# Kernel tuning notes

Hardware: AMD Instinct MI355X
Metric: run time of the kernel (lower is better)

The kernel has to match this reference:

```python
import jax, jax.numpy as jnp
import numpy as np

B, L1, L2, H = 8, 384, 384, 128


def _lin(k, out_f, in_f, scale=0.05):
    kw, kb = jax.random.split(k)
    return (jax.random.normal(kw, (out_f, in_f), jnp.float32) * scale,
            jax.random.normal(kb, (out_f,), jnp.float32) * scale)


def setup_inputs() -> dict:
    key = jax.random.key(0)
    ks = jax.random.split(key, 10)
    Wq_w, Wq_b = _lin(ks[2], H, H)
    Wup_w, Wup_b = _lin(ks[3], H, H)
    Wvp_w, Wvp_b = _lin(ks[4], H, H)
    V_w, V_b = _lin(ks[5], 1, H)
    Wg_w, Wg_b = _lin(ks[6], 2 * H, 2 * H)
    W_ih, b_ih = _lin(ks[7], 4 * H, 2 * H)
    W_hh, b_hh = _lin(ks[8], 4 * H, H)
    return {
        "x": jax.random.normal(ks[0], (B, L1, H), jnp.float32),
        "x_mask": jnp.zeros((B, L1), dtype=bool),
        "y": jax.random.normal(ks[1], (B, L2, H), jnp.float32),
        "y_mask": jnp.zeros((B, L2), dtype=bool),
        "Wq_w": Wq_w, "Wq_b": Wq_b,
        "Wup_w": Wup_w, "Wup_b": Wup_b,
        "Wvp_w": Wvp_w, "Wvp_b": Wvp_b,
        "V_w": V_w, "V_b": V_b,
        "Wg_w": Wg_w, "Wg_b": Wg_b,
        "W_ih": W_ih, "W_hh": W_hh, "b_ih": b_ih, "b_hh": b_hh,
    }


def reference(x, x_mask, y, y_mask, Wq_w, Wq_b, Wup_w, Wup_b, Wvp_w, Wvp_b,
              V_w, V_b, Wg_w, Wg_b, W_ih, W_hh, b_ih, b_hh):
    b, l1, h = x.shape
    # projections (torch Linear: x @ W.T + b)
    x_proj = x @ Wup_w.T + Wup_b                      # [B, L1, H]
    y_proj = y @ Wq_w.T + Wq_b                        # [B, L2, H]
    # source feeds a constant zero hidden state into W_vp -> just its bias
    hidden_proj = jnp.zeros((h,), x.dtype) @ Wvp_w.T + Wvp_b  # [H]
    # additive attention scores: V . tanh(xp + yp + hp)
    sum_batch = jnp.tanh(x_proj[:, :, None, :] + y_proj[:, None, :, :] + hidden_proj)  # [B,L1,L2,H]
    s = jnp.einsum('btjh,h->btj', sum_batch, V_w[0]) + V_b[0]  # [B, L1, L2]
    # sum_mask = (1 - x_mask) outer (1 - y_mask)
    xm = 1.0 - x_mask.astype(s.dtype)
    ym = 1.0 - y_mask.astype(s.dtype)
    s = s * (xm[:, :, None] * ym[:, None, :])
    s = jnp.where(y_mask[:, None, :], -jnp.inf, s)
    alpha = jax.nn.softmax(s, axis=-1)                # [B, L1, L2]
    ct = jnp.einsum('btj,bjh->bth', alpha, y)         # [B, L1, H]
    merge = jnp.concatenate([x, ct], axis=2)          # [B, L1, 2H]
    gt = jax.nn.sigmoid(merge @ Wg_w.T + Wg_b)
    lstm_in = gt * merge                              # [B, L1, 2H]
    # single-layer unidirectional LSTM (torch gate order: i, f, g, o)
    gates_x = lstm_in @ W_ih.T + b_ih                 # [B, L1, 4H]

    def step(carry, gx):
        h_t, c_t = carry
        g = gx + h_t @ W_hh.T + b_hh
        i, f, gg, o = jnp.split(g, 4, axis=-1)
        c_n = jax.nn.sigmoid(f) * c_t + jax.nn.sigmoid(i) * jnp.tanh(gg)
        h_n = jax.nn.sigmoid(o) * jnp.tanh(c_n)
        return (h_n, c_n), h_n

    init = (jnp.zeros((b, h), x.dtype), jnp.zeros((b, h), x.dtype))
    _, hs = jax.lax.scan(step, init, jnp.swapaxes(gates_x, 0, 1))  # [L1, B, H]
    return jnp.swapaxes(hs, 0, 1)                     # [B, L1, H]
```

## Files before the change

kernel.cpp:

```cpp
#include <hip/hip_runtime.h>
#include <hip/hip_bf16.h>
#include <math.h>

typedef __attribute__((ext_vector_type(4))) float  float4v;
typedef __attribute__((ext_vector_type(2))) float  float2v;
typedef __attribute__((ext_vector_type(8))) short  short8;

#define B_ 8
#define L_ 384
#define H_ 128

__device__ __forceinline__ float bflo(unsigned int u){ unsigned int t = u << 16; float f; __builtin_memcpy(&f,&t,4); return f; }
__device__ __forceinline__ unsigned short f2bf(float f){
  unsigned int t; __builtin_memcpy(&t,&f,4);
  return (unsigned short)((t + 0x7fffu + ((t>>16)&1u)) >> 16);
}
__device__ __forceinline__ float fsig(float x){ return __fdividef(1.f, 1.f + __expf(-x)); }

__device__ __forceinline__ void barrier_lds(){
  asm volatile("s_waitcnt lgkmcnt(0)\n\ts_barrier" ::: "memory");
}

template<int K>
__device__ __forceinline__ void mfma_rowgemm_body(
    unsigned short* in_s,
    const float* __restrict__ inA, const float* __restrict__ inB,
    const float* __restrict__ W, const float* __restrict__ bias,
    const float* __restrict__ bias2, float* __restrict__ out,
    int Ntotal, int act, int row0, int ob)
{
  constexpr int KP = K + 2;
  const int tid  = threadIdx.x;
  const int w    = tid >> 6;
  const int l    = tid & 63;
  const int c    = l & 15;
  const int quad = l >> 4;

  #pragma unroll
  for (int it = 0; it < K/32; ++it) {
    int idx = it*256 + tid;
    int r = idx / (K/4);
    int k = (idx % (K/4)) * 4;
    float4v f;
    if (inB != nullptr && k >= 128)
      f = *(const float4v*)(inB + (size_t)(row0+r)*128 + (k-128));
    else if (inB != nullptr)
      f = *(const float4v*)(inA + (size_t)(row0+r)*128 + k);
    else
      f = *(const float4v*)(inA + (size_t)(row0+r)*K + k);
    unsigned int p0 = (unsigned int)f2bf(f.x) | ((unsigned int)f2bf(f.y) << 16);
    unsigned int p1 = (unsigned int)f2bf(f.z) | ((unsigned int)f2bf(f.w) << 16);
    *(unsigned int*)&in_s[r*KP + k]     = p0;
    *(unsigned int*)&in_s[r*KP + k + 2] = p1;
  }

  const int n = ob + w*16 + c;
  short8 bfr[K/32];
  #pragma unroll
  for (int kt = 0; kt < K/32; ++kt) {
    const float* src = W + (size_t)n*K + kt*32 + quad*8;
    float4v f0 = *(const float4v*)(src);
    float4v f1 = *(const float4v*)(src + 4);
    short8 v;
    v[0]=(short)f2bf(f0[0]); v[1]=(short)f2bf(f0[1]); v[2]=(short)f2bf(f0[2]); v[3]=(short)f2bf(f0[3]);
    v[4]=(short)f2bf(f1[0]); v[5]=(short)f2bf(f1[1]); v[6]=(short)f2bf(f1[2]); v[7]=(short)f2bf(f1[3]);
    bfr[kt] = v;
  }
  __syncthreads();

  const float4v z4 = {0.f,0.f,0.f,0.f};
  float4v acc0 = z4, acc1 = z4;
  #pragma unroll
  for (int kt = 0; kt < K/32; ++kt) {
    short8 a0 = *(const short8*)&in_s[(c     )*KP + kt*32 + quad*8];
    short8 a1 = *(const short8*)&in_s[(16 + c)*KP + kt*32 + quad*8];
    acc0 = __builtin_amdgcn_mfma_f32_16x16x32_bf16(a0, bfr[kt], acc0, 0,0,0);
    acc1 = __builtin_amdgcn_mfma_f32_16x16x32_bf16(a1, bfr[kt], acc1, 0,0,0);
  }

  float bv = bias[n] + (bias2 ? bias2[n] : 0.f);
  #pragma unroll
  for (int mt = 0; mt < 2; ++mt) {
    float4v A = mt ? acc1 : acc0;
    #pragma unroll
    for (int r = 0; r < 4; ++r) {
      int m = mt*16 + quad*4 + r;
      float val = A[r] + bv;
      if (act == 2) {
        float mg = bflo((unsigned int)in_s[m*KP + n]);
        val = fsig(val) * mg;
      }
      if (act == 3)
        out[(size_t)(row0+m)*Ntotal + (n & 127)*4 + (n >> 7)] = val;
      else
        out[(size_t)(row0+m)*Ntotal + n] = val;
    }
  }
}

template<int K>
__global__ __launch_bounds__(256) void mfma_rowgemm_kernel(
    const float* __restrict__ inA, const float* __restrict__ inB,
    const float* __restrict__ W, const float* __restrict__ bias,
    const float* __restrict__ bias2, float* __restrict__ out,
    int Ntotal, int act)
{
  __shared__ __align__(16) unsigned short in_s[32*(K+2)];
  mfma_rowgemm_body<K>(in_s, inA, inB, W, bias, bias2, out,
                       Ntotal, act, blockIdx.x*32, blockIdx.y*64);
}

__global__ __launch_bounds__(256) void proj_mfma_kernel(
    const float* __restrict__ x, const float* __restrict__ y,
    const float* __restrict__ Wup_w, const float* __restrict__ Wup_b,
    const float* __restrict__ Wq_w, const float* __restrict__ Wq_b,
    const float* __restrict__ Wvp_b,
    float* __restrict__ xp, float* __restrict__ yp)
{
  __shared__ __align__(16) unsigned short in_s[32*130];
  int bx = blockIdx.x;
  if (bx < 192)
    mfma_rowgemm_body<128>(in_s, x, nullptr, Wup_w, Wup_b, nullptr,
                           xp, 128, 0, (bx>>1)*32, (bx&1)*64);
  else {
    bx -= 192;
    mfma_rowgemm_body<128>(in_s, y, nullptr, Wq_w, Wq_b, Wvp_b,
                           yp, 128, 0, (bx>>1)*32, (bx&1)*64);
  }
}

__global__ __launch_bounds__(256) void attn_kernel(
    const float* __restrict__ xp, const float* __restrict__ yp,
    const float* __restrict__ y, const unsigned char* __restrict__ xmask,
    const unsigned char* __restrict__ ymask, const float* __restrict__ Vw,
    const float* __restrict__ Vb, float* __restrict__ ct)
{
  __shared__ __align__(16) float xp_s[8][128];
  __shared__ __align__(16) float v2_s[128];
  __shared__ __align__(16) float yp_s[32][132];
  __shared__ __align__(16) float yc_s[32][132];
  __shared__ float xm_s[8];
  __shared__ float ym_s[32];
  __shared__ float sv_s;
  const int tid = threadIdx.x;
  const int b   = blockIdx.y;
  const int t0  = blockIdx.x * 8;
  const float C2 = 2.8853900817779268f;
  {
    int r = tid >> 5, k4 = (tid & 31) * 4;
    float4v f = *(const float4v*)(xp + ((size_t)(b*L_ + t0 + r))*H_ + k4);
    float4v g; g[0]=f[0]*C2; g[1]=f[1]*C2; g[2]=f[2]*C2; g[3]=f[3]*C2;
    *(float4v*)&xp_s[r][k4] = g;
    if (tid < 32) {
      float4v v = *(const float4v*)(Vw + tid*4);
      float4v v2; v2[0]=2.f*v[0]; v2[1]=2.f*v[1]; v2[2]=2.f*v[2]; v2[3]=2.f*v[3];
      *(float4v*)&v2_s[tid*4] = v2;
    }
    if (tid < 8) xm_s[tid] = xmask[b*L_ + t0 + tid] ? 0.f : 1.f;
  }
  __syncthreads();
  if (tid < 32) {
    float4v v = *(const float4v*)&v2_s[tid*4];
    float sm = (v[0]+v[1]) + (v[2]+v[3]);
    #pragma unroll
    for (int off = 16; off >= 1; off >>= 1) sm += __shfl_xor(sm, off);
    if (tid == 0) sv_s = 0.5f*sm + Vb[0];
  }

  float4v rp[4], ry[4];
  unsigned char ymb = 0;
  {
    #pragma unroll
    for (int it = 0; it < 4; ++it) {
      int idx = it*256 + tid; int r = idx >> 5; int k4 = (idx & 31) * 4;
      size_t base = ((size_t)(b*L_ + r))*H_ + k4;
      rp[it] = *(const float4v*)(yp + base);
      ry[it] = *(const float4v*)(y + base);
    }
    if (tid < 32) ymb = ymask[b*L_ + tid];
  }

  const int t = tid >> 5, u = tid & 31;
  float mrun = -__builtin_inff(), lrun = 0.f;
  float a0=0.f, a1=0.f, a2=0.f, a3=0.f;
  float svc = 0.f, xmv = 0.f;

  for (int c = 0; c < 12; ++c) {
    __syncthreads();
    #pragma unroll
    for (int it = 0; it < 4; ++it) {
      int idx = it*256 + tid; int r = idx >> 5; int k4 = (idx & 31) * 4;
      float4v sp; sp[0]=rp[it][0]*C2; sp[1]=rp[it][1]*C2; sp[2]=rp[it][2]*C2; sp[3]=rp[it][3]*C2;
      *(float4v*)&yp_s[r][k4] = sp;
      *(float4v*)&yc_s[r][k4] = ry[it];
    }
    if (tid < 32) ym_s[tid] = ymb ? 0.f : 1.f;
    __syncthreads();
    if (c == 0) { svc = sv_s; xmv = xm_s[t]; }
    if (c < 11) {
      #pragma unroll
      for (int it = 0; it < 4; ++it) {
        int idx = it*256 + tid; int r = idx >> 5; int k4 = (idx & 31) * 4;
        size_t base = ((size_t)(b*L_ + (c+1)*32 + r))*H_ + k4;
        rp[it] = *(const float4v*)(yp + base);
        ry[it] = *(const float4v*)(y + base);
      }
      if (tid < 32) ymb = ymask[b*L_ + (c+1)*32 + tid];
    }

    float sA = 0.f, sB = 0.f;
    {
      const float* yr = yp_s[u];
      const float* xr = xp_s[t];
      #pragma unroll 4
      for (int k = 0; k < 128; k += 4) {
        float4v yv = *(const float4v*)&yr[k];
        float4v xv = *(const float4v*)&xr[k];
        float4v vv = *(const float4v*)&v2_s[k];
        float e0 = __builtin_amdgcn_exp2f(xv[0] + yv[0]);
        sA -= vv[0] * __builtin_amdgcn_rcpf(e0 + 1.f);
        float e1 = __builtin_amdgcn_exp2f(xv[1] + yv[1]);
        sB -= vv[1] * __builtin_amdgcn_rcpf(e1 + 1.f);
        float e2 = __builtin_amdgcn_exp2f(xv[2] + yv[2]);
        sA -= vv[2] * __builtin_amdgcn_rcpf(e2 + 1.f);
        float e3 = __builtin_amdgcn_exp2f(xv[3] + yv[3]);
        sB -= vv[3] * __builtin_amdgcn_rcpf(e3 + 1.f);
      }
    }
    float ymv = ym_s[u];
    float s = (svc + sA + sB) * xmv * ymv;
    if (ymv == 0.f) s = -__builtin_inff();
    float mc = s;
    #pragma unroll
    for (int off = 16; off >= 1; off >>= 1) mc = fmaxf(mc, __shfl_xor(mc, off));
    float mnew = fmaxf(mrun, mc);
    float p  = __expf(s - mnew);
    float sc = __expf(mrun - mnew);
    float ps = p;
    #pragma unroll
    for (int off = 16; off >= 1; off >>= 1) ps += __shfl_xor(ps, off);
    lrun = lrun * sc + ps;
    mrun = mnew;
    a0 *= sc; a1 *= sc; a2 *= sc; a3 *= sc;
    #pragma unroll 8
    for (int j = 0; j < 32; ++j) {
      float pv = __shfl(p, j, 32);
      float4v yv = *(const float4v*)&yc_s[j][u*4];
      a0 += pv*yv[0]; a1 += pv*yv[1]; a2 += pv*yv[2]; a3 += pv*yv[3];
    }
  }
  float inv = __fdividef(1.f, lrun);
  float4v ov; ov[0]=a0*inv; ov[1]=a1*inv; ov[2]=a2*inv; ov[3]=a3*inv;
  *(float4v*)(ct + ((size_t)(b*L_ + t0 + t))*H_ + u*4) = ov;
}

__global__ __launch_bounds__(512) void lstm_kernel(
    const float* __restrict__ gx, const float* __restrict__ Whh,
    float* __restrict__ out)
{
  __shared__ __align__(16) unsigned short h_s[2][128];
  const int tid  = threadIdx.x;
  const int b    = blockIdx.x;
  const int w    = tid >> 6;
  const int l    = tid & 63;
  const int col  = l & 15;
  const int quad = l >> 4;

  short8 bf[4][4];
  #pragma unroll
  for (int nt = 0; nt < 4; ++nt) {
    const int n = nt*128 + w*16 + col;
    #pragma unroll
    for (int kt = 0; kt < 4; ++kt) {
      const int k0 = kt*32 + quad*8;
      const float* src = Whh + (size_t)n*H_ + k0;
      float4v f0 = *(const float4v*)(src);
      float4v f1 = *(const float4v*)(src + 4);
      short8 v;
      v[0]=(short)f2bf(f0[0]); v[1]=(short)f2bf(f0[1]); v[2]=(short)f2bf(f0[2]); v[3]=(short)f2bf(f0[3]);
      v[4]=(short)f2bf(f1[0]); v[5]=(short)f2bf(f1[1]); v[6]=(short)f2bf(f1[2]); v[7]=(short)f2bf(f1[3]);
      bf[nt][kt] = v;
    }
  }

  if (tid < 128) { h_s[0][tid] = 0; h_s[1][tid] = 0; }
  float cst = 0.f;
  const int goff = w*16 + col;
  const float* gbase = gx + (size_t)b*L_*512 + goff*4;
  float* outp = out + (size_t)b*L_*H_ + goff;
  float4v gbuf[4];
  #pragma unroll
  for (int s = 0; s < 4; ++s)
    gbuf[s] = *(const float4v*)(gbase + (size_t)s*512);
  const float4v z4 = {0.f,0.f,0.f,0.f};
  const float NL2E = -1.4426950408889634f;
  const float P2L2E = 2.8853900817779268f;
  __syncthreads();

  for (int t4 = 0; t4 < L_; t4 += 4) {
    #pragma unroll
    for (int s = 0; s < 4; ++s) {
      const int tstep = t4 + s;
      const unsigned short* hb = h_s[s & 1];
      short8 a[4];
      #pragma unroll
      for (int kt=0;kt<4;++kt) a[kt] = *(const short8*)&hb[kt*32 + quad*8];
      float4v c0 = z4, c1 = z4, c2 = z4, c3 = z4;
      #pragma unroll
      for (int kt=0;kt<4;++kt) {
        c0 = __builtin_amdgcn_mfma_f32_16x16x32_bf16(a[kt], bf[0][kt], c0, 0,0,0);
        c1 = __builtin_amdgcn_mfma_f32_16x16x32_bf16(a[kt], bf[1][kt], c1, 0,0,0);
        c2 = __builtin_amdgcn_mfma_f32_16x16x32_bf16(a[kt], bf[2][kt], c2, 0,0,0);
        c3 = __builtin_amdgcn_mfma_f32_16x16x32_bf16(a[kt], bf[3][kt], c3, 0,0,0);
      }
      float g0 = c0[0] + gbuf[s][0];
      float g1 = c1[0] + gbuf[s][1];
      float g2 = c2[0] + gbuf[s][2];
      float g3 = c3[0] + gbuf[s][3];
      if (tstep + 4 < L_)
        gbuf[s] = *(const float4v*)(gbase + (size_t)(tstep+4)*512);
      if (quad == 0) {
        float ig = __builtin_amdgcn_rcpf(1.f + __builtin_amdgcn_exp2f(NL2E*g0));
        float fg = __builtin_amdgcn_rcpf(1.f + __builtin_amdgcn_exp2f(NL2E*g1));
        float gg = 1.f - 2.f*__builtin_amdgcn_rcpf(__builtin_amdgcn_exp2f(P2L2E*g2) + 1.f);
        float og = __builtin_amdgcn_rcpf(1.f + __builtin_amdgcn_exp2f(NL2E*g3));
        cst = fg*cst + ig*gg;
        float hn = og * (1.f - 2.f*__builtin_amdgcn_rcpf(__builtin_amdgcn_exp2f(P2L2E*cst) + 1.f));
        outp[(size_t)tstep*H_] = hn;
        h_s[(s+1)&1][goff] = f2bf(hn);
      }
      barrier_lds();
    }
  }
}

extern "C" void kernel_launch(void* const* d_in, const int* in_sizes, int n_in,
                              void* d_out, int out_size, void* d_ws, size_t ws_size,
                              hipStream_t stream)
{
  (void)in_sizes; (void)n_in; (void)out_size; (void)ws_size;
  const float* x     = (const float*)d_in[0];
  const unsigned char* xm = (const unsigned char*)d_in[1];
  const float* y     = (const float*)d_in[2];
  const unsigned char* ym = (const unsigned char*)d_in[3];
  const float* Wq_w  = (const float*)d_in[4];
  const float* Wq_b  = (const float*)d_in[5];
  const float* Wup_w = (const float*)d_in[6];
  const float* Wup_b = (const float*)d_in[7];
  const float* Wvp_b = (const float*)d_in[9];
  const float* V_w   = (const float*)d_in[10];
  const float* V_b   = (const float*)d_in[11];
  const float* Wg_w  = (const float*)d_in[12];
  const float* Wg_b  = (const float*)d_in[13];
  const float* W_ih  = (const float*)d_in[14];
  const float* W_hh  = (const float*)d_in[15];
  const float* b_ih  = (const float*)d_in[16];
  const float* b_hh  = (const float*)d_in[17];
  float* out = (float*)d_out;

  float* wsf   = (float*)d_ws;
  float* xp_ws = wsf;
  float* yp_ws = xp_ws + 393216;
  float* ct_ws = yp_ws + 393216;
  float* li_ws = ct_ws + 393216;
  float* gx_ws = li_ws + 786432;

  proj_mfma_kernel<<<dim3(384),256,0,stream>>>(x, y, Wup_w, Wup_b, Wq_w, Wq_b, Wvp_b, xp_ws, yp_ws);
  attn_kernel<<<dim3(48,8),256,0,stream>>>(xp_ws, yp_ws, y, xm, ym, V_w, V_b, ct_ws);
  mfma_rowgemm_kernel<256><<<dim3(96,4),256,0,stream>>>(x, ct_ws, Wg_w, Wg_b, nullptr, li_ws, 256, 2);
  mfma_rowgemm_kernel<256><<<dim3(96,8),256,0,stream>>>(li_ws, nullptr, W_ih, b_ih, b_hh, gx_ws, 512, 3);
  lstm_kernel<<<dim3(8),512,0,stream>>>(gx_ws, W_hh, out);
}
```

Before: 364.0 us.

## Split attention over key dimension into two halves with a merge kernel

The attention kernel now launches a third grid dimension that splits the 384 keys into two halves of 192. Each half writes its unnormalized context plus running max and sum to the workspace. A new merge kernel combines the two partial softmax results. This doubles the block count so the GPU is filled better, in exchange for an extra launch and extra global traffic for the partial results.

```diff
diff --git a/kernel.cpp b/kernel.cpp
--- a/kernel.cpp
+++ b/kernel.cpp
@@ -133,7 +133,9 @@
     const float* __restrict__ xp, const float* __restrict__ yp,
     const float* __restrict__ y, const unsigned char* __restrict__ xmask,
     const unsigned char* __restrict__ ymask, const float* __restrict__ Vw,
-    const float* __restrict__ Vb, float* __restrict__ ct)
+    const float* __restrict__ Vb,
+    float* __restrict__ ctp0, float* __restrict__ ctp1,
+    float* __restrict__ ml)
 {
   __shared__ __align__(16) float xp_s[8][128];
   __shared__ __align__(16) float v2_s[128];
@@ -145,6 +147,7 @@
   const int tid = threadIdx.x;
   const int b   = blockIdx.y;
   const int t0  = blockIdx.x * 8;
+  const int jh  = blockIdx.z;
   const float C2 = 2.8853900817779268f;
   {
     int r = tid >> 5, k4 = (tid & 31) * 4;
@@ -173,11 +176,11 @@
     #pragma unroll
     for (int it = 0; it < 4; ++it) {
       int idx = it*256 + tid; int r = idx >> 5; int k4 = (idx & 31) * 4;
-      size_t base = ((size_t)(b*L_ + r))*H_ + k4;
+      size_t base = ((size_t)(b*L_ + jh*192 + r))*H_ + k4;
       rp[it] = *(const float4v*)(yp + base);
       ry[it] = *(const float4v*)(y + base);
     }
-    if (tid < 32) ymb = ymask[b*L_ + tid];
+    if (tid < 32) ymb = ymask[b*L_ + jh*192 + tid];
   }
 
   const int t = tid >> 5, u = tid & 31;
@@ -185,7 +188,7 @@
   float a0=0.f, a1=0.f, a2=0.f, a3=0.f;
   float svc = 0.f, xmv = 0.f;
 
-  for (int c = 0; c < 12; ++c) {
+  for (int c = 0; c < 6; ++c) {
     __syncthreads();
     #pragma unroll
     for (int it = 0; it < 4; ++it) {
@@ -197,15 +200,15 @@
     if (tid < 32) ym_s[tid] = ymb ? 0.f : 1.f;
     __syncthreads();
     if (c == 0) { svc = sv_s; xmv = xm_s[t]; }
-    if (c < 11) {
+    if (c < 5) {
       #pragma unroll
       for (int it = 0; it < 4; ++it) {
         int idx = it*256 + tid; int r = idx >> 5; int k4 = (idx & 31) * 4;
-        size_t base = ((size_t)(b*L_ + (c+1)*32 + r))*H_ + k4;
+        size_t base = ((size_t)(b*L_ + jh*192 + (c+1)*32 + r))*H_ + k4;
         rp[it] = *(const float4v*)(yp + base);
         ry[it] = *(const float4v*)(y + base);
       }
-      if (tid < 32) ymb = ymask[b*L_ + (c+1)*32 + tid];
+      if (tid < 32) ymb = ymask[b*L_ + jh*192 + (c+1)*32 + tid];
     }
 
     float sA = 0.f, sB = 0.f;
@@ -249,9 +252,36 @@
       a0 += pv*yv[0]; a1 += pv*yv[1]; a2 += pv*yv[2]; a3 += pv*yv[3];
     }
   }
-  float inv = __fdividef(1.f, lrun);
-  float4v ov; ov[0]=a0*inv; ov[1]=a1*inv; ov[2]=a2*inv; ov[3]=a3*inv;
-  *(float4v*)(ct + ((size_t)(b*L_ + t0 + t))*H_ + u*4) = ov;
+  const int row = b*L_ + t0 + t;
+  float* ctp = jh ? ctp1 : ctp0;
+  float4v ov; ov[0]=a0; ov[1]=a1; ov[2]=a2; ov[3]=a3;
+  *(float4v*)(ctp + (size_t)row*H_ + u*4) = ov;
+  if (u == 0) {
+    ml[(jh*2+0)*3072 + row] = mrun;
+    ml[(jh*2+1)*3072 + row] = lrun;
+  }
+}
+
+__global__ __launch_bounds__(256) void attn_merge_kernel(
+    const float* __restrict__ ctp0, const float* __restrict__ ctp1,
+    const float* __restrict__ ml, float* __restrict__ ct)
+{
+  const int tid = threadIdx.x;
+  const int row = blockIdx.x*8 + (tid >> 5);
+  const int c4  = (tid & 31) * 4;
+  float m0 = ml[row],        l0 = ml[3072 + row];
+  float m1 = ml[2*3072+row], l1 = ml[3*3072 + row];
+  float m  = fmaxf(m0, m1);
+  float e0 = __expf(m0 - m), e1 = __expf(m1 - m);
+  float inv = __fdividef(1.f, l0*e0 + l1*e1);
+  float4v v0 = *(const float4v*)(ctp0 + (size_t)row*H_ + c4);
+  float4v v1 = *(const float4v*)(ctp1 + (size_t)row*H_ + c4);
+  float4v r;
+  r[0] = (v0[0]*e0 + v1[0]*e1)*inv;
+  r[1] = (v0[1]*e0 + v1[1]*e1)*inv;
+  r[2] = (v0[2]*e0 + v1[2]*e1)*inv;
+  r[3] = (v0[3]*e0 + v1[3]*e1)*inv;
+  *(float4v*)(ct + (size_t)row*H_ + c4) = r;
 }
 
 __global__ __launch_bounds__(512) void lstm_kernel(
@@ -358,15 +388,18 @@
   const float* b_hh  = (const float*)d_in[17];
   float* out = (float*)d_out;
 
-  float* wsf   = (float*)d_ws;
-  float* xp_ws = wsf;
-  float* yp_ws = xp_ws + 393216;
-  float* ct_ws = yp_ws + 393216;
-  float* li_ws = ct_ws + 393216;
-  float* gx_ws = li_ws + 786432;
+  float* wsf    = (float*)d_ws;
+  float* xp_ws  = wsf;
+  float* yp_ws  = xp_ws + 393216;
+  float* ct_ws  = yp_ws + 393216;
+  float* li_ws  = ct_ws + 393216;
+  float* gx_ws  = li_ws + 786432;
+  float* ct2_ws = gx_ws + 1572864;
+  float* ml_ws  = ct2_ws + 393216;
 
   proj_mfma_kernel<<<dim3(384),256,0,stream>>>(x, y, Wup_w, Wup_b, Wq_w, Wq_b, Wvp_b, xp_ws, yp_ws);
-  attn_kernel<<<dim3(48,8),256,0,stream>>>(xp_ws, yp_ws, y, xm, ym, V_w, V_b, ct_ws);
+  attn_kernel<<<dim3(48,8,2),256,0,stream>>>(xp_ws, yp_ws, y, xm, ym, V_w, V_b, ct_ws, ct2_ws, ml_ws);
+  attn_merge_kernel<<<dim3(384),256,0,stream>>>(ct_ws, ct2_ws, ml_ws, ct_ws);
   mfma_rowgemm_kernel<256><<<dim3(96,4),256,0,stream>>>(x, ct_ws, Wg_w, Wg_b, nullptr, li_ws, 256, 2);
   mfma_rowgemm_kernel<256><<<dim3(96,8),256,0,stream>>>(li_ws, nullptr, W_ih, b_ih, b_hh, gx_ws, 512, 3);
   lstm_kernel<<<dim3(8),512,0,stream>>>(gx_ws, W_hh, out);
```

Result: faster. 345.4 us (-5.1%).
